# Optimization experiments

Measured on AMD Instinct MI355X. Metric: run time of the kernel, lower is better.

The kernel has to match this reference:

```python
import jax, jax.numpy as jnp
import numpy as np

DIM_GATE = 256
DIM_BIAS = 128
H = 8
D = 32
EPS = 1e-5


def _layernorm(t, gamma, beta):
    mu = jnp.mean(t, axis=-1, keepdims=True)
    var = jnp.mean(jnp.square(t - mu), axis=-1, keepdims=True)
    return (t - mu) * jax.lax.rsqrt(var + EPS) * gamma + beta


def setup_inputs() -> dict:
    key = jax.random.key(0)
    ks = jax.random.split(key, 12)
    b, l = 2, 512
    x = jax.random.normal(ks[0], (b, l, DIM_GATE), dtype=jnp.float32)
    bias = jax.random.normal(ks[1], (b, l, l, DIM_BIAS), dtype=jnp.float32)
    s_g = 1.0 / np.sqrt(DIM_GATE)
    s_b = 1.0 / np.sqrt(DIM_BIAS)
    return {
        "x": x,
        "bias": bias,
        "g_gamma": jnp.ones((DIM_GATE,), jnp.float32),
        "g_beta": jnp.zeros((DIM_GATE,), jnp.float32),
        "b_gamma": jnp.ones((DIM_BIAS,), jnp.float32),
        "b_beta": jnp.zeros((DIM_BIAS,), jnp.float32),
        "Wq": jax.random.normal(ks[2], (DIM_GATE, H * D), jnp.float32) * s_g,
        "Wk": jax.random.normal(ks[3], (DIM_GATE, H * D), jnp.float32) * s_g,
        "Wv": jax.random.normal(ks[4], (DIM_GATE, H * D), jnp.float32) * s_g,
        "Wb": jax.random.normal(ks[5], (DIM_BIAS, H), jnp.float32) * s_b,
        "Wg": jax.random.normal(ks[6], (DIM_GATE, H * D), jnp.float32) * s_g,
        "bg": jnp.zeros((H * D,), jnp.float32),
        "Wout": jax.random.normal(ks[7], (H * D, DIM_GATE), jnp.float32) * s_g,
        "bout": jnp.zeros((DIM_GATE,), jnp.float32),
    }


def reference(x, bias, g_gamma, g_beta, b_gamma, b_beta, Wq, Wk, Wv, Wb, Wg, bg, Wout, bout):
    b, l, _ = x.shape
    scaling = 1.0 / np.sqrt(D)
    xn = _layernorm(x, g_gamma, g_beta)                      # [b,l,dg]
    bn = _layernorm(bias, b_gamma, b_beta)                   # [b,l,l,db]
    q = (xn @ Wq).reshape(b, l, H, D)                        # [b,l,h,d]
    k = (xn @ Wk).reshape(b, l, H, D) * scaling
    v = (xn @ Wv).reshape(b, l, H, D)
    pair_b = bn @ Wb                                         # [b,q,k,h]
    gate = jax.nn.sigmoid(xn @ Wg + bg)                      # [b,l,h*d]
    attn = jnp.einsum('bqhd,bkhd->bqkh', q, k) + pair_b      # [b,q,k,h]
    attn = jax.nn.softmax(attn, axis=-2)                     # softmax over k
    out = jnp.einsum('bqkh,bkhd->bqhd', attn, v).reshape(b, l, H * D)
    out = gate * out
    return out @ Wout + bout
```

## Files before the change

### kernel.cpp

```cpp
#include <hip/hip_runtime.h>
#include <math.h>

#define LSEQ 512
#define DG 256
#define DB 128
#define NH 8
#define HD 32
#define EPSV 1e-5f

__global__ __launch_bounds__(256) void prep_kernel(
    const float* __restrict__ x, const float* __restrict__ g_gamma,
    const float* __restrict__ g_beta, const float* __restrict__ Wq,
    const float* __restrict__ Wk, const float* __restrict__ Wv,
    const float* __restrict__ Wg, const float* __restrict__ bg,
    float* __restrict__ q_ws, float* __restrict__ k_ws,
    float* __restrict__ v_ws, float* __restrict__ g_ws)
{
    __shared__ float xs[4][DG];
    const int t = threadIdx.x;
    const int wave = t >> 6, lane = t & 63;
    const int row0 = blockIdx.x << 2;

    {
        const int row = row0 + wave;
        const float4 xv = *(const float4*)(x + (size_t)row * DG + lane * 4);
        float s  = xv.x + xv.y + xv.z + xv.w;
        float ss = xv.x*xv.x + xv.y*xv.y + xv.z*xv.z + xv.w*xv.w;
        #pragma unroll
        for (int m = 32; m >= 1; m >>= 1) { s += __shfl_xor(s, m); ss += __shfl_xor(ss, m); }
        const float mean = s * (1.f / DG);
        const float rstd = rsqrtf(ss * (1.f / DG) - mean * mean + EPSV);
        const float4 gg = *(const float4*)(g_gamma + lane * 4);
        const float4 gb = *(const float4*)(g_beta + lane * 4);
        float4 xo;
        xo.x = (xv.x - mean) * rstd * gg.x + gb.x;
        xo.y = (xv.y - mean) * rstd * gg.y + gb.y;
        xo.z = (xv.z - mean) * rstd * gg.z + gb.z;
        xo.w = (xv.w - mean) * rstd * gg.w + gb.w;
        *(float4*)&xs[wave][lane * 4] = xo;
    }
    __syncthreads();

    float aq[4] = {0,0,0,0}, ak[4] = {0,0,0,0}, av[4] = {0,0,0,0}, ag[4] = {0,0,0,0};
    #pragma unroll 4
    for (int c = 0; c < DG; ++c) {
        const float wq = Wq[(size_t)c * DG + t];
        const float wk = Wk[(size_t)c * DG + t];
        const float wv = Wv[(size_t)c * DG + t];
        const float wg = Wg[(size_t)c * DG + t];
        #pragma unroll
        for (int r = 0; r < 4; ++r) {
            const float xr = xs[r][c];
            aq[r] = fmaf(xr, wq, aq[r]);
            ak[r] = fmaf(xr, wk, ak[r]);
            av[r] = fmaf(xr, wv, av[r]);
            ag[r] = fmaf(xr, wg, ag[r]);
        }
    }

    const float scal = 0.17677669529663687f;
    const float bgv = bg[t];
    #pragma unroll
    for (int r = 0; r < 4; ++r) {
        const size_t o = (size_t)(row0 + r) * DG + t;
        q_ws[o] = aq[r];
        k_ws[o] = ak[r] * scal;
        v_ws[o] = av[r];
        g_ws[o] = 1.f / (1.f + __expf(-(ag[r] + bgv)));
    }
}

__global__ __launch_bounds__(256) void attn_kernel(
    const float* __restrict__ bias, const float* __restrict__ b_gamma,
    const float* __restrict__ b_beta, const float* __restrict__ Wb,
    const float* __restrict__ Wout, const float* __restrict__ bout,
    const float* __restrict__ q_ws, const float* __restrict__ k_ws,
    const float* __restrict__ v_ws, const float* __restrict__ g_ws,
    float* __restrict__ out)
{
    __shared__ float logit[LSEQ * NH];
    __shared__ float q_sp[NH * 33];
    __shared__ float s1_s[NH], s0_s[NH], rden_s[NH];
    __shared__ float row_s[DG];

    const int t = threadIdx.x;
    const int bq = blockIdx.x;
    const int b = bq >> 9;

    q_sp[(t >> 5) * 33 + (t & 31)] = q_ws[(size_t)bq * DG + t];
    if (t < NH) {
        float s1 = 0.f, s0 = 0.f;
        for (int c = 0; c < DB; ++c) {
            const float w = Wb[(size_t)c * NH + t];
            s1 = fmaf(b_gamma[c], w, s1);
            s0 = fmaf(b_beta[c],  w, s0);
        }
        s1_s[t] = s1; s0_s[t] = s0;
    }
    __syncthreads();

    {
        const int h = t & 7, kk = t >> 3;
        const float* qrow = &q_sp[h * 33];
        for (int it = 0; it < 16; ++it) {
            const int k = it * 32 + kk;
            const float* kv = k_ws + ((size_t)(b * LSEQ + k)) * DG + h * HD;
            float acc = 0.f;
            #pragma unroll
            for (int d4 = 0; d4 < 8; ++d4) {
                const float4 kvv = *(const float4*)(kv + d4 * 4);
                acc = fmaf(qrow[d4*4+0], kvv.x, acc);
                acc = fmaf(qrow[d4*4+1], kvv.y, acc);
                acc = fmaf(qrow[d4*4+2], kvv.z, acc);
                acc = fmaf(qrow[d4*4+3], kvv.w, acc);
            }
            logit[k * NH + h] = acc;
        }
    }
    __syncthreads();

    {
        const int g = t >> 5, lane = t & 31;
        const int c0 = lane * 4;
        const int bit4 = (lane >> 4) & 1, bit3 = (lane >> 3) & 1, bit2 = (lane >> 2) & 1;
        const int h_mine = bit4 * 4 + bit3 * 2 + bit2;
        const bool writer = (lane & 3) == 0;
        const float s1m = s1_s[h_mine], s0m = s0_s[h_mine];

        const float4 gm4 = *(const float4*)(b_gamma + c0);
        const float gam[4] = {gm4.x, gm4.y, gm4.z, gm4.w};
        float gw[4][8];
        #pragma unroll
        for (int j = 0; j < 4; ++j) {
            const float4 wa = *(const float4*)(Wb + (size_t)(c0 + j) * NH);
            const float4 wb2 = *(const float4*)(Wb + (size_t)(c0 + j) * NH + 4);
            gw[j][0] = gam[j]*wa.x;  gw[j][1] = gam[j]*wa.y;
            gw[j][2] = gam[j]*wa.z;  gw[j][3] = gam[j]*wa.w;
            gw[j][4] = gam[j]*wb2.x; gw[j][5] = gam[j]*wb2.y;
            gw[j][6] = gam[j]*wb2.z; gw[j][7] = gam[j]*wb2.w;
        }

        const float* brow_base = bias + (size_t)bq * LSEQ * DB;
        for (int it = 0; it < 64; ++it) {
            const int k = it * 8 + g;
            const float4 bv = *(const float4*)(brow_base + (size_t)k * DB + c0);
            float s  = bv.x + bv.y + bv.z + bv.w;
            float ss = fmaf(bv.x, bv.x, fmaf(bv.y, bv.y, fmaf(bv.z, bv.z, bv.w * bv.w)));
            #pragma unroll
            for (int m = 16; m >= 1; m >>= 1) { s += __shfl_xor(s, m); ss += __shfl_xor(ss, m); }
            const float mean = s * (1.f / DB);
            const float rstd = rsqrtf(ss * (1.f / DB) - mean * mean + EPSV);

            float dot[8];
            #pragma unroll
            for (int h = 0; h < 8; ++h)
                dot[h] = fmaf(bv.x, gw[0][h], fmaf(bv.y, gw[1][h],
                         fmaf(bv.z, gw[2][h], bv.w * gw[3][h])));

            float m4[4];
            #pragma unroll
            for (int j = 0; j < 4; ++j) {
                const float keep = bit4 ? dot[4 + j] : dot[j];
                const float send = bit4 ? dot[j] : dot[4 + j];
                m4[j] = keep + __shfl_xor(send, 16);
            }
            float m2[2];
            #pragma unroll
            for (int j = 0; j < 2; ++j) {
                const float keep = bit3 ? m4[2 + j] : m4[j];
                const float send = bit3 ? m4[j] : m4[2 + j];
                m2[j] = keep + __shfl_xor(send, 8);
            }
            float m1;
            {
                const float keep = bit2 ? m2[1] : m2[0];
                const float send = bit2 ? m2[0] : m2[1];
                m1 = keep + __shfl_xor(send, 4);
            }
            m1 += __shfl_xor(m1, 2);
            m1 += __shfl_xor(m1, 1);

            if (writer)
                logit[k * NH + h_mine] += rstd * (m1 - mean * s1m) + s0m;
        }
    }
    __syncthreads();

    {
        const int h = t >> 5, lane = t & 31;
        float mx = -1e30f;
        for (int j = 0; j < 16; ++j) mx = fmaxf(mx, logit[(lane + j * 32) * NH + h]);
        #pragma unroll
        for (int m = 16; m >= 1; m >>= 1) mx = fmaxf(mx, __shfl_xor(mx, m));
        float s = 0.f;
        for (int j = 0; j < 16; ++j) {
            const int idx = (lane + j * 32) * NH + h;
            const float e = __expf(logit[idx] - mx);
            logit[idx] = e;
            s += e;
        }
        #pragma unroll
        for (int m = 16; m >= 1; m >>= 1) s += __shfl_xor(s, m);
        if (lane == 0) rden_s[h] = 1.f / s;
    }
    __syncthreads();

    {
        const int h = t >> 5;
        float acc = 0.f;
        const float* vb = v_ws + (size_t)(b * LSEQ) * DG + t;
        #pragma unroll 8
        for (int k = 0; k < LSEQ; ++k)
            acc = fmaf(logit[k * NH + h], vb[(size_t)k * DG], acc);
        row_s[t] = acc * rden_s[h] * g_ws[(size_t)bq * DG + t];
    }
    __syncthreads();

    {
        float o = bout[t];
        #pragma unroll 4
        for (int c = 0; c < DG; ++c)
            o = fmaf(row_s[c], Wout[(size_t)c * DG + t], o);
        out[(size_t)bq * DG + t] = o;
    }
}

extern "C" void kernel_launch(void* const* d_in, const int* in_sizes, int n_in,
                              void* d_out, int out_size, void* d_ws, size_t ws_size,
                              hipStream_t stream)
{
    const float* x       = (const float*)d_in[0];
    const float* bias    = (const float*)d_in[1];
    const float* g_gamma = (const float*)d_in[2];
    const float* g_beta  = (const float*)d_in[3];
    const float* b_gamma = (const float*)d_in[4];
    const float* b_beta  = (const float*)d_in[5];
    const float* Wq      = (const float*)d_in[6];
    const float* Wk      = (const float*)d_in[7];
    const float* Wv      = (const float*)d_in[8];
    const float* Wb      = (const float*)d_in[9];
    const float* Wg      = (const float*)d_in[10];
    const float* bg      = (const float*)d_in[11];
    const float* Wout    = (const float*)d_in[12];
    const float* bout    = (const float*)d_in[13];
    float* out = (float*)d_out;

    float* ws   = (float*)d_ws;
    float* q_ws = ws;
    float* k_ws = ws + 262144;
    float* v_ws = ws + 2 * 262144;
    float* g_ws = ws + 3 * 262144;

    hipLaunchKernelGGL(prep_kernel, dim3(256), dim3(256), 0, stream,
                       x, g_gamma, g_beta, Wq, Wk, Wv, Wg, bg,
                       q_ws, k_ws, v_ws, g_ws);
    hipLaunchKernelGGL(attn_kernel, dim3(1024), dim3(256), 0, stream,
                       bias, b_gamma, b_beta, Wb, Wout, bout,
                       q_ws, k_ws, v_ws, g_ws, out);
}
```

Before: 590.9 us.

## Widen attention blocks to 1024 threads and split reductions across k-chunks

```diff
diff --git a/kernel.cpp b/kernel.cpp
--- a/kernel.cpp
+++ b/kernel.cpp
@@ -6,6 +6,7 @@
 #define DB 128
 #define NH 8
 #define HD 32
+#define LP 520
 #define EPSV 1e-5f
 
 __global__ __launch_bounds__(256) void prep_kernel(
@@ -16,12 +17,12 @@
     float* __restrict__ q_ws, float* __restrict__ k_ws,
     float* __restrict__ v_ws, float* __restrict__ g_ws)
 {
-    __shared__ float xs[4][DG];
+    __shared__ float xs[2][DG];
     const int t = threadIdx.x;
     const int wave = t >> 6, lane = t & 63;
-    const int row0 = blockIdx.x << 2;
-
-    {
+    const int row0 = blockIdx.x << 1;
+
+    if (wave < 2) {
         const int row = row0 + wave;
         const float4 xv = *(const float4*)(x + (size_t)row * DG + lane * 4);
         float s  = xv.x + xv.y + xv.z + xv.w;
@@ -41,36 +42,34 @@
     }
     __syncthreads();
 
-    float aq[4] = {0,0,0,0}, ak[4] = {0,0,0,0}, av[4] = {0,0,0,0}, ag[4] = {0,0,0,0};
-    #pragma unroll 4
+    float aq0=0, aq1=0, ak0=0, ak1=0, av0=0, av1=0, ag0=0, ag1=0;
+    #pragma unroll 8
     for (int c = 0; c < DG; ++c) {
         const float wq = Wq[(size_t)c * DG + t];
         const float wk = Wk[(size_t)c * DG + t];
         const float wv = Wv[(size_t)c * DG + t];
         const float wg = Wg[(size_t)c * DG + t];
-        #pragma unroll
-        for (int r = 0; r < 4; ++r) {
-            const float xr = xs[r][c];
-            aq[r] = fmaf(xr, wq, aq[r]);
-            ak[r] = fmaf(xr, wk, ak[r]);
-            av[r] = fmaf(xr, wv, av[r]);
-            ag[r] = fmaf(xr, wg, ag[r]);
-        }
+        const float x0 = xs[0][c], x1 = xs[1][c];
+        aq0 = fmaf(x0, wq, aq0);  aq1 = fmaf(x1, wq, aq1);
+        ak0 = fmaf(x0, wk, ak0);  ak1 = fmaf(x1, wk, ak1);
+        av0 = fmaf(x0, wv, av0);  av1 = fmaf(x1, wv, av1);
+        ag0 = fmaf(x0, wg, ag0);  ag1 = fmaf(x1, wg, ag1);
     }
 
     const float scal = 0.17677669529663687f;
     const float bgv = bg[t];
-    #pragma unroll
-    for (int r = 0; r < 4; ++r) {
-        const size_t o = (size_t)(row0 + r) * DG + t;
-        q_ws[o] = aq[r];
-        k_ws[o] = ak[r] * scal;
-        v_ws[o] = av[r];
-        g_ws[o] = 1.f / (1.f + __expf(-(ag[r] + bgv)));
+    {
+        const size_t o0 = (size_t)row0 * DG + t;
+        const size_t o1 = o0 + DG;
+        q_ws[o0] = aq0;               q_ws[o1] = aq1;
+        k_ws[o0] = ak0 * scal;        k_ws[o1] = ak1 * scal;
+        v_ws[o0] = av0;               v_ws[o1] = av1;
+        g_ws[o0] = 1.f / (1.f + __expf(-(ag0 + bgv)));
+        g_ws[o1] = 1.f / (1.f + __expf(-(ag1 + bgv)));
     }
 }
 
-__global__ __launch_bounds__(256) void attn_kernel(
+__global__ __launch_bounds__(1024) void attn_kernel(
     const float* __restrict__ bias, const float* __restrict__ b_gamma,
     const float* __restrict__ b_beta, const float* __restrict__ Wb,
     const float* __restrict__ Wout, const float* __restrict__ bout,
@@ -78,33 +77,43 @@
     const float* __restrict__ v_ws, const float* __restrict__ g_ws,
     float* __restrict__ out)
 {
-    __shared__ float logit[LSEQ * NH];
+    __shared__ float lg[NH * LP];
+    __shared__ float pb[NH * LP];
     __shared__ float q_sp[NH * 33];
     __shared__ float s1_s[NH], s0_s[NH], rden_s[NH];
+    __shared__ float ps[4][DG];
     __shared__ float row_s[DG];
 
     const int t = threadIdx.x;
     const int bq = blockIdx.x;
     const int b = bq >> 9;
 
-    q_sp[(t >> 5) * 33 + (t & 31)] = q_ws[(size_t)bq * DG + t];
-    if (t < NH) {
+    if (t < DG) {
+        q_sp[(t >> 5) * 33 + (t & 31)] = q_ws[(size_t)bq * DG + t];
+    } else if (t < 2 * DG) {
+        const int tt = t - DG;
+        const int h = tt >> 5, l = tt & 31, c0 = l * 4;
         float s1 = 0.f, s0 = 0.f;
-        for (int c = 0; c < DB; ++c) {
-            const float w = Wb[(size_t)c * NH + t];
-            s1 = fmaf(b_gamma[c], w, s1);
-            s0 = fmaf(b_beta[c],  w, s0);
-        }
-        s1_s[t] = s1; s0_s[t] = s0;
+        #pragma unroll
+        for (int j = 0; j < 4; ++j) {
+            const float w = Wb[(size_t)(c0 + j) * NH + h];
+            s1 = fmaf(b_gamma[c0 + j], w, s1);
+            s0 = fmaf(b_beta[c0 + j],  w, s0);
+        }
+        #pragma unroll
+        for (int m = 16; m >= 1; m >>= 1) { s1 += __shfl_xor(s1, m); s0 += __shfl_xor(s0, m); }
+        if (l == 0) { s1_s[h] = s1; s0_s[h] = s0; }
     }
     __syncthreads();
 
     {
         const int h = t & 7, kk = t >> 3;
         const float* qrow = &q_sp[h * 33];
-        for (int it = 0; it < 16; ++it) {
-            const int k = it * 32 + kk;
-            const float* kv = k_ws + ((size_t)(b * LSEQ + k)) * DG + h * HD;
+        const float* kbase = k_ws + (size_t)(b * LSEQ) * DG + h * HD;
+        #pragma unroll
+        for (int j = 0; j < 4; ++j) {
+            const int k = kk + j * 128;
+            const float* kv = kbase + (size_t)k * DG;
             float acc = 0.f;
             #pragma unroll
             for (int d4 = 0; d4 < 8; ++d4) {
@@ -114,17 +123,16 @@
                 acc = fmaf(qrow[d4*4+2], kvv.z, acc);
                 acc = fmaf(qrow[d4*4+3], kvv.w, acc);
             }
-            logit[k * NH + h] = acc;
-        }
-    }
-    __syncthreads();
-
-    {
-        const int g = t >> 5, lane = t & 31;
-        const int c0 = lane * 4;
-        const int bit4 = (lane >> 4) & 1, bit3 = (lane >> 3) & 1, bit2 = (lane >> 2) & 1;
+            lg[h * LP + k] = acc;
+        }
+    }
+
+    {
+        const int G = t >> 5, l = t & 31;
+        const int c0 = l * 4;
+        const int bit4 = (l >> 4) & 1, bit3 = (l >> 3) & 1, bit2 = (l >> 2) & 1;
         const int h_mine = bit4 * 4 + bit3 * 2 + bit2;
-        const bool writer = (lane & 3) == 0;
+        const bool writer = (l & 3) == 0;
         const float s1m = s1_s[h_mine], s0m = s0_s[h_mine];
 
         const float4 gm4 = *(const float4*)(b_gamma + c0);
@@ -140,88 +148,140 @@
             gw[j][6] = gam[j]*wb2.z; gw[j][7] = gam[j]*wb2.w;
         }
 
-        const float* brow_base = bias + (size_t)bq * LSEQ * DB;
-        for (int it = 0; it < 64; ++it) {
-            const int k = it * 8 + g;
-            const float4 bv = *(const float4*)(brow_base + (size_t)k * DB + c0);
-            float s  = bv.x + bv.y + bv.z + bv.w;
-            float ss = fmaf(bv.x, bv.x, fmaf(bv.y, bv.y, fmaf(bv.z, bv.z, bv.w * bv.w)));
-            #pragma unroll
-            for (int m = 16; m >= 1; m >>= 1) { s += __shfl_xor(s, m); ss += __shfl_xor(ss, m); }
-            const float mean = s * (1.f / DB);
-            const float rstd = rsqrtf(ss * (1.f / DB) - mean * mean + EPSV);
-
-            float dot[8];
-            #pragma unroll
-            for (int h = 0; h < 8; ++h)
-                dot[h] = fmaf(bv.x, gw[0][h], fmaf(bv.y, gw[1][h],
-                         fmaf(bv.z, gw[2][h], bv.w * gw[3][h])));
-
-            float m4[4];
+        const float* bb = bias + (size_t)bq * LSEQ * DB;
+        for (int it = 0; it < 8; ++it) {
+            const int ka = it * 32 + G;
+            const int kb = ka + 256;
+            const float4 va = *(const float4*)(bb + (size_t)ka * DB + c0);
+            const float4 vb2 = *(const float4*)(bb + (size_t)kb * DB + c0);
+
+            float sa  = va.x + va.y + va.z + va.w;
+            float sb  = vb2.x + vb2.y + vb2.z + vb2.w;
+            float ssa = fmaf(va.x, va.x, fmaf(va.y, va.y, fmaf(va.z, va.z, va.w * va.w)));
+            float ssb = fmaf(vb2.x, vb2.x, fmaf(vb2.y, vb2.y, fmaf(vb2.z, vb2.z, vb2.w * vb2.w)));
+            #pragma unroll
+            for (int m = 16; m >= 1; m >>= 1) {
+                sa += __shfl_xor(sa, m);   ssa += __shfl_xor(ssa, m);
+                sb += __shfl_xor(sb, m);   ssb += __shfl_xor(ssb, m);
+            }
+            const float mean_a = sa * (1.f / DB);
+            const float mean_b = sb * (1.f / DB);
+            const float rstd_a = rsqrtf(ssa * (1.f / DB) - mean_a * mean_a + EPSV);
+            const float rstd_b = rsqrtf(ssb * (1.f / DB) - mean_b * mean_b + EPSV);
+
+            float da[8], db2[8];
+            #pragma unroll
+            for (int h = 0; h < 8; ++h) {
+                da[h]  = fmaf(va.x, gw[0][h], fmaf(va.y, gw[1][h],
+                         fmaf(va.z, gw[2][h], va.w * gw[3][h])));
+                db2[h] = fmaf(vb2.x, gw[0][h], fmaf(vb2.y, gw[1][h],
+                         fmaf(vb2.z, gw[2][h], vb2.w * gw[3][h])));
+            }
+
+            float a4[4], b4[4];
             #pragma unroll
             for (int j = 0; j < 4; ++j) {
-                const float keep = bit4 ? dot[4 + j] : dot[j];
-                const float send = bit4 ? dot[j] : dot[4 + j];
-                m4[j] = keep + __shfl_xor(send, 16);
-            }
-            float m2[2];
+                float ka_ = bit4 ? da[4 + j] : da[j];
+                float sa_ = bit4 ? da[j] : da[4 + j];
+                a4[j] = ka_ + __shfl_xor(sa_, 16);
+                float kb_ = bit4 ? db2[4 + j] : db2[j];
+                float sb_ = bit4 ? db2[j] : db2[4 + j];
+                b4[j] = kb_ + __shfl_xor(sb_, 16);
+            }
+            float a2[2], b2[2];
             #pragma unroll
             for (int j = 0; j < 2; ++j) {
-                const float keep = bit3 ? m4[2 + j] : m4[j];
-                const float send = bit3 ? m4[j] : m4[2 + j];
-                m2[j] = keep + __shfl_xor(send, 8);
-            }
-            float m1;
+                float ka_ = bit3 ? a4[2 + j] : a4[j];
+                float sa_ = bit3 ? a4[j] : a4[2 + j];
+                a2[j] = ka_ + __shfl_xor(sa_, 8);
+                float kb_ = bit3 ? b4[2 + j] : b4[j];
+                float sb_ = bit3 ? b4[j] : b4[2 + j];
+                b2[j] = kb_ + __shfl_xor(sb_, 8);
+            }
+            float a1, b1;
             {
-                const float keep = bit2 ? m2[1] : m2[0];
-                const float send = bit2 ? m2[0] : m2[1];
-                m1 = keep + __shfl_xor(send, 4);
-            }
-            m1 += __shfl_xor(m1, 2);
-            m1 += __shfl_xor(m1, 1);
-
-            if (writer)
-                logit[k * NH + h_mine] += rstd * (m1 - mean * s1m) + s0m;
-        }
-    }
-    __syncthreads();
-
-    {
-        const int h = t >> 5, lane = t & 31;
+                float ka_ = bit2 ? a2[1] : a2[0];
+                float sa_ = bit2 ? a2[0] : a2[1];
+                a1 = ka_ + __shfl_xor(sa_, 4);
+                float kb_ = bit2 ? b2[1] : b2[0];
+                float sb_ = bit2 ? b2[0] : b2[1];
+                b1 = kb_ + __shfl_xor(sb_, 4);
+            }
+            a1 += __shfl_xor(a1, 2);  b1 += __shfl_xor(b1, 2);
+            a1 += __shfl_xor(a1, 1);  b1 += __shfl_xor(b1, 1);
+
+            if (writer) {
+                pb[h_mine * LP + ka] = rstd_a * (a1 - mean_a * s1m) + s0m;
+                pb[h_mine * LP + kb] = rstd_b * (b1 - mean_b * s1m) + s0m;
+            }
+        }
+    }
+    __syncthreads();
+
+    if (t < 256) {
+        const int h = t >> 5, l = t & 31;
+        float* lrow = &lg[h * LP];
+        const float* prow = &pb[h * LP];
         float mx = -1e30f;
-        for (int j = 0; j < 16; ++j) mx = fmaxf(mx, logit[(lane + j * 32) * NH + h]);
+        #pragma unroll
+        for (int j = 0; j < 16; ++j) {
+            const int k = l + j * 32;
+            const float v = lrow[k] + prow[k];
+            lrow[k] = v;
+            mx = fmaxf(mx, v);
+        }
         #pragma unroll
         for (int m = 16; m >= 1; m >>= 1) mx = fmaxf(mx, __shfl_xor(mx, m));
         float s = 0.f;
+        #pragma unroll
         for (int j = 0; j < 16; ++j) {
-            const int idx = (lane + j * 32) * NH + h;
-            const float e = __expf(logit[idx] - mx);
-            logit[idx] = e;
+            const int k = l + j * 32;
+            const float e = __expf(lrow[k] - mx);
+            lrow[k] = e;
             s += e;
         }
         #pragma unroll
         for (int m = 16; m >= 1; m >>= 1) s += __shfl_xor(s, m);
-        if (lane == 0) rden_s[h] = 1.f / s;
-    }
-    __syncthreads();
-
-    {
-        const int h = t >> 5;
-        float acc = 0.f;
-        const float* vb = v_ws + (size_t)(b * LSEQ) * DG + t;
+        if (l == 0) rden_s[h] = 1.f / s;
+    }
+    __syncthreads();
+
+    {
+        const int c = t & 255, kq = t >> 8;
+        const int h = c >> 5;
+        const float* vb = v_ws + ((size_t)(b * LSEQ) + kq * 128) * DG + c;
+        const float* lgb = &lg[h * LP + kq * 128];
+        float a0 = 0.f, a1 = 0.f;
         #pragma unroll 8
-        for (int k = 0; k < LSEQ; ++k)
-            acc = fmaf(logit[k * NH + h], vb[(size_t)k * DG], acc);
-        row_s[t] = acc * rden_s[h] * g_ws[(size_t)bq * DG + t];
-    }
-    __syncthreads();
-
-    {
-        float o = bout[t];
-        #pragma unroll 4
-        for (int c = 0; c < DG; ++c)
-            o = fmaf(row_s[c], Wout[(size_t)c * DG + t], o);
-        out[(size_t)bq * DG + t] = o;
+        for (int i = 0; i < 128; i += 2) {
+            a0 = fmaf(lgb[i],     vb[(size_t)i * DG],       a0);
+            a1 = fmaf(lgb[i + 1], vb[(size_t)(i + 1) * DG], a1);
+        }
+        ps[kq][c] = a0 + a1;
+    }
+    __syncthreads();
+    if (t < DG) {
+        const float s = (ps[0][t] + ps[1][t] + ps[2][t] + ps[3][t])
+                        * rden_s[t >> 5] * g_ws[(size_t)bq * DG + t];
+        row_s[t] = s;
+    }
+    __syncthreads();
+
+    {
+        const int c = t & 255, qc = t >> 8;
+        const float* wob = Wout + (size_t)(qc * 64) * DG + c;
+        const float* rs = &row_s[qc * 64];
+        float a0 = 0.f, a1 = 0.f;
+        #pragma unroll 8
+        for (int i = 0; i < 64; i += 2) {
+            a0 = fmaf(rs[i],     wob[(size_t)i * DG],       a0);
+            a1 = fmaf(rs[i + 1], wob[(size_t)(i + 1) * DG], a1);
+        }
+        ps[qc][c] = a0 + a1;
+    }
+    __syncthreads();
+    if (t < DG) {
+        out[(size_t)bq * DG + t] = ps[0][t] + ps[1][t] + ps[2][t] + ps[3][t] + bout[t];
     }
 }
 
@@ -251,10 +311,10 @@
     float* v_ws = ws + 2 * 262144;
     float* g_ws = ws + 3 * 262144;
 
-    hipLaunchKernelGGL(prep_kernel, dim3(256), dim3(256), 0, stream,
+    hipLaunchKernelGGL(prep_kernel, dim3(512), dim3(256), 0, stream,
                        x, g_gamma, g_beta, Wq, Wk, Wv, Wg, bg,
                        q_ws, k_ws, v_ws, g_ws);
-    hipLaunchKernelGGL(attn_kernel, dim3(1024), dim3(256), 0, stream,
+    hipLaunchKernelGGL(attn_kernel, dim3(1024), dim3(1024), 0, stream,
                        bias, b_gamma, b_beta, Wb, Wout, bout,
                        q_ws, k_ws, v_ws, g_ws, out);
 }
```

Result: faster. 561.5 us (-5.0%).

## Split pair-bias into MFMA kernel with async LDS staging; batch two queries per attention block

Applied to the files above, without the earlier changes.

```diff
diff --git a/kernel.cpp b/kernel.cpp
--- a/kernel.cpp
+++ b/kernel.cpp
@@ -7,6 +7,19 @@
 #define NH 8
 #define HD 32
 #define EPSV 1e-5f
+#define LP2 516
+
+typedef __attribute__((ext_vector_type(8))) short bf16x8;
+typedef __attribute__((ext_vector_type(4))) float f32x4;
+
+__device__ __forceinline__ unsigned short f2bf(float x) {
+    unsigned int u = __float_as_uint(x);
+    u += 0x7FFFu + ((u >> 16) & 1u);
+    return (unsigned short)(u >> 16);
+}
+__device__ __forceinline__ float bf2f(unsigned short h) {
+    return __uint_as_float(((unsigned int)h) << 16);
+}
 
 __global__ __launch_bounds__(256) void prep_kernel(
     const float* __restrict__ x, const float* __restrict__ g_gamma,
@@ -70,158 +83,227 @@
     }
 }
 
-__global__ __launch_bounds__(256) void attn_kernel(
+__global__ __launch_bounds__(256) void pairb_kernel(
     const float* __restrict__ bias, const float* __restrict__ b_gamma,
     const float* __restrict__ b_beta, const float* __restrict__ Wb,
-    const float* __restrict__ Wout, const float* __restrict__ bout,
-    const float* __restrict__ q_ws, const float* __restrict__ k_ws,
-    const float* __restrict__ v_ws, const float* __restrict__ g_ws,
-    float* __restrict__ out)
+    float* __restrict__ pair_ws)
 {
-    __shared__ float logit[LSEQ * NH];
-    __shared__ float q_sp[NH * 33];
-    __shared__ float s1_s[NH], s0_s[NH], rden_s[NH];
-    __shared__ float row_s[DG];
-
+    __shared__ float lds[4 * 2 * 2048];
     const int t = threadIdx.x;
+    const int w = t >> 6, l = t & 63;
+    const int n = l & 15, quad = l >> 4;
     const int bq = blockIdx.x;
-    const int b = bq >> 9;
-
-    q_sp[(t >> 5) * 33 + (t & 31)] = q_ws[(size_t)bq * DG + t];
-    if (t < NH) {
-        float s1 = 0.f, s0 = 0.f;
-        for (int c = 0; c < DB; ++c) {
-            const float w = Wb[(size_t)c * NH + t];
-            s1 = fmaf(b_gamma[c], w, s1);
-            s0 = fmaf(b_beta[c],  w, s0);
-        }
-        s1_s[t] = s1; s0_s[t] = s0;
-    }
-    __syncthreads();
-
-    {
-        const int h = t & 7, kk = t >> 3;
-        const float* qrow = &q_sp[h * 33];
-        for (int it = 0; it < 16; ++it) {
-            const int k = it * 32 + kk;
-            const float* kv = k_ws + ((size_t)(b * LSEQ + k)) * DG + h * HD;
-            float acc = 0.f;
+
+    bf16x8 gwhi[4], gwlo[4];
+    float S1 = 0.f, S0 = 0.f;
+    #pragma unroll
+    for (int ks = 0; ks < 4; ++ks) {
+        #pragma unroll
+        for (int j = 0; j < 8; ++j) {
+            const int c = ks * 32 + quad * 8 + j;
+            const float wb = (n < 8) ? Wb[c * 8 + n] : 0.f;
+            const float wv = b_gamma[c] * wb;
+            S1 += wv;
+            S0 += b_beta[c] * wb;
+            unsigned short hi = f2bf(wv);
+            unsigned short lo = f2bf(wv - bf2f(hi));
+            if (n == 8) { hi = 0x3F80; lo = 0; }
+            gwhi[ks][j] = (short)hi;
+            gwlo[ks][j] = (short)lo;
+        }
+    }
+    S1 += __shfl_xor(S1, 16); S1 += __shfl_xor(S1, 32);
+    S0 += __shfl_xor(S0, 16); S0 += __shfl_xor(S0, 32);
+
+    float* myl = lds + w * 4096;
+    const size_t rowbase = (size_t)bq * LSEQ + w * 16;
+
+    auto stage = [&](int tt, int buf) {
+        const float* src = bias + (rowbase + (size_t)tt * 64) * DB;
+        float* dst = myl + buf * 2048;
+        #pragma unroll
+        for (int i = 0; i < 8; ++i) {
+            __builtin_amdgcn_global_load_lds(
+                (const __attribute__((address_space(1))) void*)(src + i * 256 + l * 4),
+                (__attribute__((address_space(3))) void*)(dst + i * 256 + l * 4),
+                16, 0, 0);
+        }
+    };
+
+    auto compute = [&](int tt, int buf) {
+        const float* d = myl + buf * 2048 + n * 128 + quad * 8;
+        f32x4 acc = {0.f, 0.f, 0.f, 0.f};
+        float ssq = 0.f;
+        #pragma unroll
+        for (int ks = 0; ks < 4; ++ks) {
+            const float4 x0 = *(const float4*)(d + ks * 32);
+            const float4 x1 = *(const float4*)(d + ks * 32 + 4);
+            ssq = fmaf(x0.x,x0.x, fmaf(x0.y,x0.y, fmaf(x0.z,x0.z, fmaf(x0.w,x0.w, ssq))));
+            ssq = fmaf(x1.x,x1.x, fmaf(x1.y,x1.y, fmaf(x1.z,x1.z, fmaf(x1.w,x1.w, ssq))));
+            const float xsv[8] = {x0.x,x0.y,x0.z,x0.w,x1.x,x1.y,x1.z,x1.w};
+            bf16x8 ahi, alo;
             #pragma unroll
-            for (int d4 = 0; d4 < 8; ++d4) {
-                const float4 kvv = *(const float4*)(kv + d4 * 4);
-                acc = fmaf(qrow[d4*4+0], kvv.x, acc);
-                acc = fmaf(qrow[d4*4+1], kvv.y, acc);
-                acc = fmaf(qrow[d4*4+2], kvv.z, acc);
-                acc = fmaf(qrow[d4*4+3], kvv.w, acc);
+            for (int j = 0; j < 8; ++j) {
+                const unsigned short hi = f2bf(xsv[j]);
+                ahi[j] = (short)hi;
+                alo[j] = (short)f2bf(xsv[j] - bf2f(hi));
             }
-            logit[k * NH + h] = acc;
-        }
-    }
-    __syncthreads();
-
-    {
-        const int g = t >> 5, lane = t & 31;
-        const int c0 = lane * 4;
-        const int bit4 = (lane >> 4) & 1, bit3 = (lane >> 3) & 1, bit2 = (lane >> 2) & 1;
-        const int h_mine = bit4 * 4 + bit3 * 2 + bit2;
-        const bool writer = (lane & 3) == 0;
-        const float s1m = s1_s[h_mine], s0m = s0_s[h_mine];
-
-        const float4 gm4 = *(const float4*)(b_gamma + c0);
-        const float gam[4] = {gm4.x, gm4.y, gm4.z, gm4.w};
-        float gw[4][8];
-        #pragma unroll
-        for (int j = 0; j < 4; ++j) {
-            const float4 wa = *(const float4*)(Wb + (size_t)(c0 + j) * NH);
-            const float4 wb2 = *(const float4*)(Wb + (size_t)(c0 + j) * NH + 4);
-            gw[j][0] = gam[j]*wa.x;  gw[j][1] = gam[j]*wa.y;
-            gw[j][2] = gam[j]*wa.z;  gw[j][3] = gam[j]*wa.w;
-            gw[j][4] = gam[j]*wb2.x; gw[j][5] = gam[j]*wb2.y;
-            gw[j][6] = gam[j]*wb2.z; gw[j][7] = gam[j]*wb2.w;
-        }
-
-        const float* brow_base = bias + (size_t)bq * LSEQ * DB;
-        for (int it = 0; it < 64; ++it) {
-            const int k = it * 8 + g;
-            const float4 bv = *(const float4*)(brow_base + (size_t)k * DB + c0);
-            float s  = bv.x + bv.y + bv.z + bv.w;
-            float ss = fmaf(bv.x, bv.x, fmaf(bv.y, bv.y, fmaf(bv.z, bv.z, bv.w * bv.w)));
+            acc = __builtin_amdgcn_mfma_f32_16x16x32_bf16(ahi, gwhi[ks], acc, 0, 0, 0);
+            acc = __builtin_amdgcn_mfma_f32_16x16x32_bf16(alo, gwhi[ks], acc, 0, 0, 0);
+            acc = __builtin_amdgcn_mfma_f32_16x16x32_bf16(ahi, gwlo[ks], acc, 0, 0, 0);
+        }
+        ssq += __shfl_xor(ssq, 16);
+        ssq += __shfl_xor(ssq, 32);
+        float* pout = pair_ws + (rowbase + (size_t)tt * 64 + quad * 4) * NH + n;
+        #pragma unroll
+        for (int reg = 0; reg < 4; ++reg) {
+            const float sumr = __uint_as_float((unsigned)__builtin_amdgcn_ds_bpermute(
+                (quad * 16 + 8) * 4, (int)__float_as_uint(acc[reg])));
+            const float ssqr = __uint_as_float((unsigned)__builtin_amdgcn_ds_bpermute(
+                (quad * 4 + reg) * 4, (int)__float_as_uint(ssq)));
+            const float mean = sumr * (1.f / DB);
+            const float var  = ssqr * (1.f / DB) - mean * mean;
+            const float rstd = rsqrtf(var + EPSV);
+            const float p = rstd * (acc[reg] - mean * S1) + S0;
+            if (n < NH) pout[reg * NH] = p;
+        }
+    };
+
+    stage(0, 0);
+    stage(1, 1);
+    asm volatile("s_waitcnt vmcnt(8)" ::: "memory");
+    compute(0, 0);
+    for (int tt = 1; tt < 7; ++tt) {
+        stage(tt + 1, (tt + 1) & 1);
+        asm volatile("s_waitcnt vmcnt(12)" ::: "memory");
+        compute(tt, tt & 1);
+    }
+    asm volatile("s_waitcnt vmcnt(4)" ::: "memory");
+    compute(7, 1);
+}
+
+__global__ __launch_bounds__(512) void attn_kernel(
+    const float* __restrict__ pair_ws, const float* __restrict__ Wout,
+    const float* __restrict__ bout, const float* __restrict__ q_ws,
+    const float* __restrict__ k_ws, const float* __restrict__ v_ws,
+    const float* __restrict__ g_ws, float* __restrict__ out)
+{
+    __shared__ float lg[2 * NH * LP2];
+    __shared__ float q_s[2 * DG];
+    __shared__ float ps[4 * 2 * 64 * 4];
+    __shared__ float row_s[2 * DG];
+    __shared__ float rden[16];
+
+    const int t = threadIdx.x;
+    const int b = blockIdx.x >> 8;
+    const int q0 = (blockIdx.x & 255) * 2;
+
+    {
+        const float* pbase = pair_ws + ((size_t)(b * LSEQ + q0)) * LSEQ * NH;
+        #pragma unroll
+        for (int r = 0; r < 4; ++r) {
+            const int f = r * 512 + t;
+            const float4 pv = *(const float4*)(pbase + (size_t)f * 4);
+            const int q = f >> 10;
+            const int o = (f * 4) & 4095;
+            const int k = o >> 3, hb = o & 7;
+            float* dst = lg + (q * NH + hb) * LP2 + k;
+            dst[0] = pv.x; dst[LP2] = pv.y; dst[2*LP2] = pv.z; dst[3*LP2] = pv.w;
+        }
+        q_s[t] = q_ws[((size_t)(b * LSEQ + q0)) * DG + t];
+    }
+    __syncthreads();
+
+    {
+        const int h = t >> 6, kk = t & 63;
+        const float* kb = k_ws + ((size_t)(b * LSEQ)) * DG + h * HD;
+        const float* qp0 = q_s + h * HD;
+        const float* qp1 = q_s + DG + h * HD;
+        for (int j = 0; j < 8; ++j) {
+            const int k = kk + j * 64;
+            const float* kr = kb + (size_t)k * DG;
+            float a0 = 0.f, a1 = 0.f;
             #pragma unroll
-            for (int m = 16; m >= 1; m >>= 1) { s += __shfl_xor(s, m); ss += __shfl_xor(ss, m); }
-            const float mean = s * (1.f / DB);
-            const float rstd = rsqrtf(ss * (1.f / DB) - mean * mean + EPSV);
-
-            float dot[8];
-            #pragma unroll
-            for (int h = 0; h < 8; ++h)
-                dot[h] = fmaf(bv.x, gw[0][h], fmaf(bv.y, gw[1][h],
-                         fmaf(bv.z, gw[2][h], bv.w * gw[3][h])));
-
-            float m4[4];
-            #pragma unroll
-            for (int j = 0; j < 4; ++j) {
-                const float keep = bit4 ? dot[4 + j] : dot[j];
-                const float send = bit4 ? dot[j] : dot[4 + j];
-                m4[j] = keep + __shfl_xor(send, 16);
+            for (int c = 0; c < 8; ++c) {
+                const float4 kv = *(const float4*)(kr + c * 4);
+                const float4 qa = *(const float4*)(qp0 + c * 4);
+                const float4 qb = *(const float4*)(qp1 + c * 4);
+                a0 = fmaf(kv.x, qa.x, fmaf(kv.y, qa.y, fmaf(kv.z, qa.z, fmaf(kv.w, qa.w, a0))));
+                a1 = fmaf(kv.x, qb.x, fmaf(kv.y, qb.y, fmaf(kv.z, qb.z, fmaf(kv.w, qb.w, a1))));
             }
-            float m2[2];
-            #pragma unroll
-            for (int j = 0; j < 2; ++j) {
-                const float keep = bit3 ? m4[2 + j] : m4[j];
-                const float send = bit3 ? m4[j] : m4[2 + j];
-                m2[j] = keep + __shfl_xor(send, 8);
-            }
-            float m1;
-            {
-                const float keep = bit2 ? m2[1] : m2[0];
-                const float send = bit2 ? m2[0] : m2[1];
-                m1 = keep + __shfl_xor(send, 4);
-            }
-            m1 += __shfl_xor(m1, 2);
-            m1 += __shfl_xor(m1, 1);
-
-            if (writer)
-                logit[k * NH + h_mine] += rstd * (m1 - mean * s1m) + s0m;
-        }
-    }
-    __syncthreads();
-
-    {
-        const int h = t >> 5, lane = t & 31;
+            lg[(0 * NH + h) * LP2 + k] += a0;
+            lg[(1 * NH + h) * LP2 + k] += a1;
+        }
+    }
+    __syncthreads();
+
+    {
+        const int qh = t >> 5, l32 = t & 31;
+        float* lrow = lg + qh * LP2;
         float mx = -1e30f;
-        for (int j = 0; j < 16; ++j) mx = fmaxf(mx, logit[(lane + j * 32) * NH + h]);
+        #pragma unroll
+        for (int i = 0; i < 16; ++i) mx = fmaxf(mx, lrow[l32 + i * 32]);
         #pragma unroll
         for (int m = 16; m >= 1; m >>= 1) mx = fmaxf(mx, __shfl_xor(mx, m));
         float s = 0.f;
-        for (int j = 0; j < 16; ++j) {
-            const int idx = (lane + j * 32) * NH + h;
-            const float e = __expf(logit[idx] - mx);
-            logit[idx] = e;
+        #pragma unroll
+        for (int i = 0; i < 16; ++i) {
+            const int k = l32 + i * 32;
+            const float e = __expf(lrow[k] - mx);
+            lrow[k] = e;
             s += e;
         }
         #pragma unroll
         for (int m = 16; m >= 1; m >>= 1) s += __shfl_xor(s, m);
-        if (lane == 0) rden_s[h] = 1.f / s;
-    }
-    __syncthreads();
-
-    {
-        const int h = t >> 5;
-        float acc = 0.f;
-        const float* vb = v_ws + (size_t)(b * LSEQ) * DG + t;
-        #pragma unroll 8
-        for (int k = 0; k < LSEQ; ++k)
-            acc = fmaf(logit[k * NH + h], vb[(size_t)k * DG], acc);
-        row_s[t] = acc * rden_s[h] * g_ws[(size_t)bq * DG + t];
-    }
-    __syncthreads();
-
-    {
-        float o = bout[t];
+        if (l32 == 0) rden[qh] = 1.f / s;
+    }
+    __syncthreads();
+
+    {
+        const int q = t >> 8, s4 = (t >> 6) & 3, c4 = t & 63;
+        const int h = c4 >> 3;
+        const float* vb = v_ws + ((size_t)(b * LSEQ + s4 * 128)) * DG + c4 * 4;
+        const float* prow = lg + (q * NH + h) * LP2 + s4 * 128;
+        float4 a = {0.f, 0.f, 0.f, 0.f};
+        #pragma unroll 4
+        for (int i = 0; i < 128; ++i) {
+            const float p = prow[i];
+            const float4 vv = *(const float4*)(vb + (size_t)i * DG);
+            a.x = fmaf(p, vv.x, a.x);
+            a.y = fmaf(p, vv.y, a.y);
+            a.z = fmaf(p, vv.z, a.z);
+            a.w = fmaf(p, vv.w, a.w);
+        }
+        *(float4*)&ps[((s4 * 2 + q) * 64 + c4) * 4] = a;
+    }
+    __syncthreads();
+    if (t < 128) {
+        const int q = t >> 6, c4 = t & 63, h = c4 >> 3;
+        float4 a = *(const float4*)&ps[((0 * 2 + q) * 64 + c4) * 4];
+        #pragma unroll
+        for (int s4 = 1; s4 < 4; ++s4) {
+            const float4 p4 = *(const float4*)&ps[((s4 * 2 + q) * 64 + c4) * 4];
+            a.x += p4.x; a.y += p4.y; a.z += p4.z; a.w += p4.w;
+        }
+        const float sc = rden[q * NH + h];
+        const float4 g4 = *(const float4*)(g_ws + ((size_t)(b * LSEQ + q0 + q)) * DG + c4 * 4);
+        float* rs = row_s + q * DG + c4 * 4;
+        rs[0] = a.x * sc * g4.x;
+        rs[1] = a.y * sc * g4.y;
+        rs[2] = a.z * sc * g4.z;
+        rs[3] = a.w * sc * g4.w;
+    }
+    __syncthreads();
+
+    {
+        const int q = t >> 8, co = t & 255;
+        const float* rs = row_s + q * DG;
+        const float* wo = Wout + co;
+        float a = 0.f;
         #pragma unroll 4
         for (int c = 0; c < DG; ++c)
-            o = fmaf(row_s[c], Wout[(size_t)c * DG + t], o);
-        out[(size_t)bq * DG + t] = o;
+            a = fmaf(rs[c], wo[(size_t)c * DG], a);
+        out[((size_t)(b * LSEQ + q0 + q)) * DG + co] = a + bout[co];
     }
 }
 
@@ -245,16 +327,18 @@
     const float* bout    = (const float*)d_in[13];
     float* out = (float*)d_out;
 
-    float* ws   = (float*)d_ws;
-    float* q_ws = ws;
-    float* k_ws = ws + 262144;
-    float* v_ws = ws + 2 * 262144;
-    float* g_ws = ws + 3 * 262144;
+    float* ws      = (float*)d_ws;
+    float* q_ws    = ws;
+    float* k_ws    = ws + 262144;
+    float* v_ws    = ws + 2 * 262144;
+    float* g_ws    = ws + 3 * 262144;
+    float* pair_ws = ws + 4 * 262144;
 
     hipLaunchKernelGGL(prep_kernel, dim3(256), dim3(256), 0, stream,
                        x, g_gamma, g_beta, Wq, Wk, Wv, Wg, bg,
                        q_ws, k_ws, v_ws, g_ws);
-    hipLaunchKernelGGL(attn_kernel, dim3(1024), dim3(256), 0, stream,
-                       bias, b_gamma, b_beta, Wb, Wout, bout,
-                       q_ws, k_ws, v_ws, g_ws, out);
-}
+    hipLaunchKernelGGL(pairb_kernel, dim3(1024), dim3(256), 0, stream,
+                       bias, b_gamma, b_beta, Wb, pair_ws);
+    hipLaunchKernelGGL(attn_kernel, dim3(512), dim3(512), 0, stream,
+                       pair_ws, Wout, bout, q_ws, k_ws, v_ws, g_ws, out);
+}
```

Result: faster. 534.8 us (-9.5%).
